# Optimization experiments

Hardware: AMD Instinct MI355X
Metric: run time of the kernel (lower is better)

Reference implementation:

```python
import jax, jax.numpy as jnp
import numpy as np

B, S_NEW, DIM = 32, 1, 4096
H, KV, HD = 32, 8, 128          # query heads, kv heads, head_dim
PREV = 2048                      # tokens already in the KV cache


def setup_inputs() -> dict:
    key = jax.random.key(0)
    ks = jax.random.split(key, 8)
    return {
        "x": jax.random.normal(ks[0], (B, S_NEW, DIM), jnp.float32),
        "wq": jax.random.normal(ks[1], (DIM, H * HD), jnp.float32) * 0.02,
        "wk": jax.random.normal(ks[2], (DIM, KV * HD), jnp.float32) * 0.02,
        "wv": jax.random.normal(ks[3], (DIM, KV * HD), jnp.float32) * 0.02,
        "wo": jax.random.normal(ks[4], (H * HD, DIM), jnp.float32) * 0.02,
        "cache_k": jax.random.normal(ks[5], (B, PREV, KV, HD), jnp.float32),
        "cache_v": jax.random.normal(ks[6], (B, PREV, KV, HD), jnp.float32),
        "freqs": jax.random.normal(ks[7], (S_NEW, HD // 2), jnp.float32),  # rotary angles (angle of freqs_cis)
    }


def _apply_rope(t, cos, sin):
    # t: [b, s, h, hd]; interleaved pairs as in torch.view_as_complex
    a = t[..., 0::2]
    b = t[..., 1::2]
    c = cos[None, :, None, :]
    s = sin[None, :, None, :]
    ra = a * c - b * s
    rb = a * s + b * c
    return jnp.stack([ra, rb], axis=-1).reshape(t.shape)


def reference(x, wq, wk, wv, wo, cache_k, cache_v, freqs):
    b, s, _ = x.shape  # s == 1 (decode)
    xq = (x @ wq).reshape(b, s, H, HD)
    xk = (x @ wk).reshape(b, s, KV, HD)
    xv = (x @ wv).reshape(b, s, KV, HD)

    cos, sin = jnp.cos(freqs), jnp.sin(freqs)
    xq = _apply_rope(xq, cos, sin)
    xk = _apply_rope(xk, cos, sin)

    # KV-cache append (update_cache_decode)
    k_full = jnp.concatenate([cache_k, xk], axis=1)  # [b, PREV+1, KV, hd]
    v_full = jnp.concatenate([cache_v, xv], axis=1)

    # GQA attention without materializing the expanded cache
    g = H // KV
    q = xq.reshape(b, KV, g, HD)  # s == 1 folded away
    scale = 1.0 / jnp.sqrt(jnp.asarray(HD, x.dtype))
    scores = jnp.einsum("bkgd,bskd->bkgs", q, k_full) * scale  # [b, KV, g, PREV+1]
    attn = jax.nn.softmax(scores, axis=-1)
    out = jnp.einsum("bkgs,bskd->bkgd", attn, v_full)  # [b, KV, g, hd]
    out = out.reshape(b, s, H * HD)
    return out @ wo
```

## Files before the change

kernel.cpp:

```cpp
#include <hip/hip_runtime.h>


#define WS_P1   0
#define WS_PA   0
#define WS_QKV  6291456
#define WS_ATTN 6488064
#define WS_P2   6619136

__global__ __launch_bounds__(256) void gemm_skinny(
    const float* __restrict__ X,
    const float* __restrict__ W0, int e0, int ld0,
    const float* __restrict__ W1, int e1, int ld1,
    const float* __restrict__ W2, int ld2,
    float* __restrict__ P, int Ntot)
{
    __shared__ float x_t[128][36];
    __shared__ float2 red[128][33];

    const int nb = blockIdx.x * 256;
    const float* W; int ld, noff;
    if (nb < e0)      { W = W0; ld = ld0; noff = 0;  }
    else if (nb < e1) { W = W1; ld = ld1; noff = e0; }
    else              { W = W2; ld = ld2; noff = e1; }

    const int k0  = blockIdx.y * 128;
    const int tid = threadIdx.x;
    const int cp  = tid & 127;
    const int kg  = tid >> 7;
    const int nn  = nb - noff + cp * 2;

    #pragma unroll
    for (int i = 0; i < 16; ++i) {
        int idx = tid + i * 256;
        int bb = idx >> 7, kk = idx & 127;
        x_t[kk][bb] = X[(size_t)bb * 4096 + k0 + kk];
    }
    __syncthreads();

    float2 acc[32];
    #pragma unroll
    for (int b = 0; b < 32; ++b) { acc[b].x = 0.f; acc[b].y = 0.f; }

    const float* Wp = W + (size_t)k0 * ld + nn;
    for (int kk0 = kg * 64; kk0 < kg * 64 + 64; kk0 += 8) {
        float2 w[8];
        #pragma unroll
        for (int u = 0; u < 8; ++u)
            w[u] = *(const float2*)&Wp[(size_t)(kk0 + u) * ld];
        #pragma unroll
        for (int u = 0; u < 8; ++u) {
            const float* xr = x_t[kk0 + u];
            #pragma unroll
            for (int bq = 0; bq < 8; ++bq) {
                float4 xv = *(const float4*)&xr[bq * 4];
                acc[bq*4+0].x += xv.x * w[u].x; acc[bq*4+0].y += xv.x * w[u].y;
                acc[bq*4+1].x += xv.y * w[u].x; acc[bq*4+1].y += xv.y * w[u].y;
                acc[bq*4+2].x += xv.z * w[u].x; acc[bq*4+2].y += xv.z * w[u].y;
                acc[bq*4+3].x += xv.w * w[u].x; acc[bq*4+3].y += xv.w * w[u].y;
            }
        }
    }

    if (kg == 1) {
        #pragma unroll
        for (int b = 0; b < 32; ++b) red[cp][b] = acc[b];
    }
    __syncthreads();
    if (kg == 0) {
        const int ks = blockIdx.y;
        #pragma unroll
        for (int b = 0; b < 32; ++b) {
            float2 o = red[cp][b];
            float2 v; v.x = acc[b].x + o.x; v.y = acc[b].y + o.y;
            *(float2*)&P[((size_t)ks * 32 + b) * Ntot + nb + cp * 2] = v;
        }
    }
}

__global__ __launch_bounds__(128) void reduce_rope(
    const float* __restrict__ P, const float* __restrict__ freqs,
    float* __restrict__ qkv)
{
    int t = blockIdx.x * 128 + threadIdx.x;
    int b = t / 3072;
    int cp = t - b * 3072;
    int n = cp * 2;
    float sx = 0.f, sy = 0.f;
    #pragma unroll
    for (int ks = 0; ks < 32; ++ks) {
        float2 v = *(const float2*)&P[((size_t)ks * 32 + b) * 6144 + n];
        sx += v.x; sy += v.y;
    }
    if (n < 5120) {
        int d = n & 127;
        float fr = freqs[d >> 1];
        float c = cosf(fr), s = sinf(fr);
        float ra = sx * c - sy * s;
        float rb = sx * s + sy * c;
        if (n < 4096) {
            const float sc = 0.08838834764831845f;
            ra *= sc; rb *= sc;
        }
        sx = ra; sy = rb;
    }
    float2 o; o.x = sx; o.y = sy;
    *(float2*)&qkv[(size_t)b * 6144 + n] = o;
}

__global__ __launch_bounds__(256, 8) void attn_split(
    const float* __restrict__ qkv,
    const float* __restrict__ ck, const float* __restrict__ cv,
    float* __restrict__ pa)
{
    __shared__ float sbuf[4096];
    __shared__ float pm[4], pl[4];

    const int blk = blockIdx.x;
    const int c   = blk & 7;
    const int kv  = (blk >> 3) & 7;
    const int b   = blk >> 6;
    const int tid = threadIdx.x;
    const int wave = tid >> 6, lane = tid & 63;
    const int psub = (lane >> 4) & 3, dl = lane & 15;
    const int s0 = c * 256;
    const bool last = (c == 7);

    float q[4][8];
    {
        const float* qb = qkv + (size_t)b * 6144 + kv * 512 + dl * 8;
        #pragma unroll
        for (int h = 0; h < 4; ++h) {
            float4 a = *(const float4*)&qb[h * 128];
            float4 e = *(const float4*)&qb[h * 128 + 4];
            q[h][0]=a.x; q[h][1]=a.y; q[h][2]=a.z; q[h][3]=a.w;
            q[h][4]=e.x; q[h][5]=e.y; q[h][6]=e.z; q[h][7]=e.w;
        }
    }

    if (last && tid < 16) {
        const float* kr = qkv + (size_t)b * 6144 + 4096 + kv * 128 + dl * 8;
        float4 k0 = *(const float4*)kr;
        float4 k1 = *(const float4*)(kr + 4);
        float p[4];
        #pragma unroll
        for (int h = 0; h < 4; ++h) {
            p[h] = q[h][0]*k0.x + q[h][1]*k0.y + q[h][2]*k0.z + q[h][3]*k0.w
                 + q[h][4]*k1.x + q[h][5]*k1.y + q[h][6]*k1.z + q[h][7]*k1.w;
        }
        #pragma unroll
        for (int off = 1; off < 16; off <<= 1) {
            #pragma unroll
            for (int h = 0; h < 4; ++h) p[h] += __shfl_xor(p[h], off);
        }
        if (dl == 0) {
            #pragma unroll
            for (int h = 0; h < 4; ++h) sbuf[h * 260 + 256] = p[h];
        }
    }

    const float* kbase = ck + (((size_t)b * 2048 + s0) * 8 + kv) * 128;
    const int srow = wave * 4 + psub;
    for (int it0 = 0; it0 < 16; it0 += 4) {
        float4 kA[4][2];
        #pragma unroll
        for (int u = 0; u < 4; ++u) {
            const float* kr = kbase + (size_t)((it0 + u) * 16 + srow) * 1024 + dl * 8;
            kA[u][0] = *(const float4*)kr;
            kA[u][1] = *(const float4*)(kr + 4);
        }
        #pragma unroll
        for (int u = 0; u < 4; ++u) {
            int s = (it0 + u) * 16 + srow;
            float p[4];
            #pragma unroll
            for (int h = 0; h < 4; ++h) {
                p[h] = q[h][0]*kA[u][0].x + q[h][1]*kA[u][0].y
                     + q[h][2]*kA[u][0].z + q[h][3]*kA[u][0].w
                     + q[h][4]*kA[u][1].x + q[h][5]*kA[u][1].y
                     + q[h][6]*kA[u][1].z + q[h][7]*kA[u][1].w;
            }
            #pragma unroll
            for (int off = 1; off < 16; off <<= 1) {
                #pragma unroll
                for (int h = 0; h < 4; ++h) p[h] += __shfl_xor(p[h], off);
            }
            if (dl == 0) {
                #pragma unroll
                for (int h = 0; h < 4; ++h) sbuf[h * 260 + s] = p[h];
            }
        }
    }
    __syncthreads();

    {
        const int h = wave;
        const int nrow = last ? 257 : 256;
        float m = -1e30f;
        for (int s = lane; s < nrow; s += 64) m = fmaxf(m, sbuf[h * 260 + s]);
        #pragma unroll
        for (int off = 1; off < 64; off <<= 1) m = fmaxf(m, __shfl_xor(m, off));
        float sum = 0.f;
        for (int s = lane; s < nrow; s += 64) {
            float p = __expf(sbuf[h * 260 + s] - m);
            sbuf[h * 260 + s] = p;
            sum += p;
        }
        #pragma unroll
        for (int off = 1; off < 64; off <<= 1) sum += __shfl_xor(sum, off);
        if (lane == 0) { pm[h] = m; pl[h] = sum; }
    }
    __syncthreads();

    const int grp = tid >> 5, l32 = tid & 31, d4 = l32 * 4;
    float4 acc[4];
    #pragma unroll
    for (int hh = 0; hh < 4; ++hh) { acc[hh].x=0.f; acc[hh].y=0.f; acc[hh].z=0.f; acc[hh].w=0.f; }
    const float* vbase = cv + (((size_t)b * 2048 + s0) * 8 + kv) * 128;
    for (int it = 0; it < 8; ++it) {
        float4 vv[4];
        float pp[4][4];
        #pragma unroll
        for (int j = 0; j < 4; ++j) {
            int s = it * 32 + j * 8 + grp;
            vv[j] = *(const float4*)&vbase[(size_t)s * 1024 + d4];
        }
        #pragma unroll
        for (int j = 0; j < 4; ++j) {
            int s = it * 32 + j * 8 + grp;
            #pragma unroll
            for (int hh = 0; hh < 4; ++hh) pp[j][hh] = sbuf[hh * 260 + s];
        }
        #pragma unroll
        for (int j = 0; j < 4; ++j) {
            #pragma unroll
            for (int hh = 0; hh < 4; ++hh) {
                acc[hh].x += pp[j][hh] * vv[j].x;
                acc[hh].y += pp[j][hh] * vv[j].y;
                acc[hh].z += pp[j][hh] * vv[j].z;
                acc[hh].w += pp[j][hh] * vv[j].w;
            }
        }
    }
    if (last && grp == 0) {
        const float* vr = qkv + (size_t)b * 6144 + 5120 + kv * 128;
        float4 v = *(const float4*)&vr[d4];
        #pragma unroll
        for (int hh = 0; hh < 4; ++hh) {
            float p = sbuf[hh * 260 + 256];
            acc[hh].x += p * v.x; acc[hh].y += p * v.y;
            acc[hh].z += p * v.z; acc[hh].w += p * v.w;
        }
    }
    __syncthreads();

    #pragma unroll
    for (int hh = 0; hh < 4; ++hh)
        *(float4*)&sbuf[grp * 512 + hh * 128 + d4] = acc[hh];
    __syncthreads();

    float* rec = pa + (size_t)blk * 520;
    for (int t = tid; t < 512; t += 256) {
        int hh = t >> 7, d = t & 127;
        float v = 0.f;
        #pragma unroll
        for (int g = 0; g < 8; ++g) v += sbuf[g * 512 + hh * 128 + d];
        rec[8 + hh * 128 + d] = v;
    }
    if (tid < 4) { rec[tid] = pm[tid]; rec[4 + tid] = pl[tid]; }
}

__global__ __launch_bounds__(128) void attn_combine(
    const float* __restrict__ pa, float* __restrict__ ao)
{
    __shared__ float w_[8][4];
    const int g = blockIdx.x;
    const int b = g >> 3, kv = g & 7;
    const int d = threadIdx.x;
    const float* base = pa + (size_t)(b * 64 + kv * 8) * 520;

    if (d < 4) {
        float M = -1e30f;
        #pragma unroll
        for (int c = 0; c < 8; ++c)
            M = fmaxf(M, base[(size_t)c * 520 + d]);
        float L = 0.f;
        float e[8];
        #pragma unroll
        for (int c = 0; c < 8; ++c) {
            e[c] = __expf(base[(size_t)c * 520 + d] - M);
            L += base[(size_t)c * 520 + 4 + d] * e[c];
        }
        float inv = 1.0f / L;
        #pragma unroll
        for (int c = 0; c < 8; ++c) w_[c][d] = e[c] * inv;
    }
    __syncthreads();

    #pragma unroll
    for (int h = 0; h < 4; ++h) {
        float v = 0.f;
        #pragma unroll
        for (int c = 0; c < 8; ++c)
            v += base[(size_t)c * 520 + 8 + h * 128 + d] * w_[c][h];
        ao[(size_t)g * 512 + h * 128 + d] = v;
    }
}

__global__ __launch_bounds__(128) void reduce_out(
    const float* __restrict__ P, float* __restrict__ out)
{
    int t = blockIdx.x * 128 + threadIdx.x;
    int b = t >> 11;
    int cp = t & 2047;
    int n = cp * 2;
    float sx = 0.f, sy = 0.f;
    #pragma unroll
    for (int ks = 0; ks < 32; ++ks) {
        float2 v = *(const float2*)&P[((size_t)ks * 32 + b) * 4096 + n];
        sx += v.x; sy += v.y;
    }
    float2 o; o.x = sx; o.y = sy;
    *(float2*)&out[(size_t)b * 4096 + n] = o;
}

extern "C" void kernel_launch(void* const* d_in, const int* in_sizes, int n_in,
                              void* d_out, int out_size, void* d_ws, size_t ws_size,
                              hipStream_t stream) {
    const float* x  = (const float*)d_in[0];
    const float* wq = (const float*)d_in[1];
    const float* wk = (const float*)d_in[2];
    const float* wv = (const float*)d_in[3];
    const float* wo = (const float*)d_in[4];
    const float* ck = (const float*)d_in[5];
    const float* cv = (const float*)d_in[6];
    const float* fr = (const float*)d_in[7];
    float* out = (float*)d_out;
    float* ws  = (float*)d_ws;

    float* P1   = ws + WS_P1;
    float* PA   = ws + WS_PA;
    float* qkv  = ws + WS_QKV;
    float* attn = ws + WS_ATTN;
    float* P2   = ws + WS_P2;

    dim3 g1(24, 32);
    gemm_skinny<<<g1, 256, 0, stream>>>(x, wq, 4096, 4096, wk, 5120, 1024,
                                        wv, 1024, P1, 6144);
    reduce_rope<<<768, 128, 0, stream>>>(P1, fr, qkv);
    attn_split<<<2048, 256, 0, stream>>>(qkv, ck, cv, PA);
    attn_combine<<<256, 128, 0, stream>>>(PA, attn);
    dim3 g4(16, 32);
    gemm_skinny<<<g4, 256, 0, stream>>>(attn, wo, 4096, 4096, wo, 4096, 4096,
                                        wo, 4096, P2, 4096);
    reduce_out<<<512, 128, 0, stream>>>(P2, out);
}
```

Before: 216.7 us.

## Split fused attention into separate scores, softmax and PV kernels

Replaces the single split-KV attention kernel, which did online softmax per chunk and rescaled chunks in the combine step, with three kernels. The first writes raw QK scores to global memory over finer chunks, the second computes the exact global softmax per (batch, kv-head) and stores its normalisation, and the third does the PV accumulation, scaled by the stored inverse sum. This simplifies the combine step and gives the scores kernel more parallelism. The cost is two extra kernel launches and an extra round trip of scores through global memory.

```diff
diff --git a/kernel.cpp b/kernel.cpp
--- a/kernel.cpp
+++ b/kernel.cpp
@@ -2,10 +2,12 @@
 
 
 #define WS_P1   0
-#define WS_PA   0
 #define WS_QKV  6291456
 #define WS_ATTN 6488064
 #define WS_P2   6619136
+#define WS_SC   10813440
+#define WS_LINV 12914688
+#define WS_PA   12915712
 
 __global__ __launch_bounds__(256) void gemm_skinny(
     const float* __restrict__ X,
@@ -107,23 +109,19 @@
     *(float2*)&qkv[(size_t)b * 6144 + n] = o;
 }
 
-__global__ __launch_bounds__(256, 8) void attn_split(
+__global__ __launch_bounds__(256) void attn_scores(
     const float* __restrict__ qkv,
-    const float* __restrict__ ck, const float* __restrict__ cv,
-    float* __restrict__ pa)
-{
-    __shared__ float sbuf[4096];
-    __shared__ float pm[4], pl[4];
-
+    const float* __restrict__ ck,
+    float* __restrict__ sc)
+{
     const int blk = blockIdx.x;
-    const int c   = blk & 7;
-    const int kv  = (blk >> 3) & 7;
-    const int b   = blk >> 6;
+    const int c   = blk & 15;
+    const int kv  = (blk >> 4) & 7;
+    const int b   = blk >> 7;
     const int tid = threadIdx.x;
     const int wave = tid >> 6, lane = tid & 63;
     const int psub = (lane >> 4) & 3, dl = lane & 15;
-    const int s0 = c * 256;
-    const bool last = (c == 7);
+    const int s0 = c * 128;
 
     float q[4][8];
     {
@@ -137,40 +135,20 @@
         }
     }
 
-    if (last && tid < 16) {
-        const float* kr = qkv + (size_t)b * 6144 + 4096 + kv * 128 + dl * 8;
-        float4 k0 = *(const float4*)kr;
-        float4 k1 = *(const float4*)(kr + 4);
-        float p[4];
-        #pragma unroll
-        for (int h = 0; h < 4; ++h) {
-            p[h] = q[h][0]*k0.x + q[h][1]*k0.y + q[h][2]*k0.z + q[h][3]*k0.w
-                 + q[h][4]*k1.x + q[h][5]*k1.y + q[h][6]*k1.z + q[h][7]*k1.w;
-        }
-        #pragma unroll
-        for (int off = 1; off < 16; off <<= 1) {
-            #pragma unroll
-            for (int h = 0; h < 4; ++h) p[h] += __shfl_xor(p[h], off);
-        }
-        if (dl == 0) {
-            #pragma unroll
-            for (int h = 0; h < 4; ++h) sbuf[h * 260 + 256] = p[h];
-        }
-    }
-
+    float* scb = sc + (size_t)(b * 8 + kv) * 8208;
     const float* kbase = ck + (((size_t)b * 2048 + s0) * 8 + kv) * 128;
     const int srow = wave * 4 + psub;
-    for (int it0 = 0; it0 < 16; it0 += 4) {
-        float4 kA[4][2];
-        #pragma unroll
-        for (int u = 0; u < 4; ++u) {
+
+    for (int it0 = 0; it0 < 8; it0 += 2) {
+        float4 kA[2][2];
+        #pragma unroll
+        for (int u = 0; u < 2; ++u) {
             const float* kr = kbase + (size_t)((it0 + u) * 16 + srow) * 1024 + dl * 8;
             kA[u][0] = *(const float4*)kr;
             kA[u][1] = *(const float4*)(kr + 4);
         }
         #pragma unroll
-        for (int u = 0; u < 4; ++u) {
-            int s = (it0 + u) * 16 + srow;
+        for (int u = 0; u < 2; ++u) {
             float p[4];
             #pragma unroll
             for (int h = 0; h < 4; ++h) {
@@ -185,124 +163,184 @@
                 for (int h = 0; h < 4; ++h) p[h] += __shfl_xor(p[h], off);
             }
             if (dl == 0) {
-                #pragma unroll
-                for (int h = 0; h < 4; ++h) sbuf[h * 260 + s] = p[h];
+                int s = s0 + (it0 + u) * 16 + srow;
+                float4 o; o.x = p[0]; o.y = p[1]; o.z = p[2]; o.w = p[3];
+                *(float4*)&scb[(size_t)s * 4] = o;
             }
         }
     }
-    __syncthreads();
-
-    {
-        const int h = wave;
-        const int nrow = last ? 257 : 256;
-        float m = -1e30f;
-        for (int s = lane; s < nrow; s += 64) m = fmaxf(m, sbuf[h * 260 + s]);
-        #pragma unroll
-        for (int off = 1; off < 64; off <<= 1) m = fmaxf(m, __shfl_xor(m, off));
-        float sum = 0.f;
-        for (int s = lane; s < nrow; s += 64) {
-            float p = __expf(sbuf[h * 260 + s] - m);
-            sbuf[h * 260 + s] = p;
-            sum += p;
-        }
-        #pragma unroll
-        for (int off = 1; off < 64; off <<= 1) sum += __shfl_xor(sum, off);
-        if (lane == 0) { pm[h] = m; pl[h] = sum; }
-    }
-    __syncthreads();
-
+
+    if (c == 15 && wave == 0 && psub == 0) {
+        const float* kr = qkv + (size_t)b * 6144 + 4096 + kv * 128 + dl * 8;
+        float4 k0 = *(const float4*)kr;
+        float4 k1 = *(const float4*)(kr + 4);
+        float p[4];
+        #pragma unroll
+        for (int h = 0; h < 4; ++h) {
+            p[h] = q[h][0]*k0.x + q[h][1]*k0.y + q[h][2]*k0.z + q[h][3]*k0.w
+                 + q[h][4]*k1.x + q[h][5]*k1.y + q[h][6]*k1.z + q[h][7]*k1.w;
+        }
+        #pragma unroll
+        for (int off = 1; off < 16; off <<= 1) {
+            #pragma unroll
+            for (int h = 0; h < 4; ++h) p[h] += __shfl_xor(p[h], off);
+        }
+        if (dl == 0) {
+            float4 o; o.x = p[0]; o.y = p[1]; o.z = p[2]; o.w = p[3];
+            *(float4*)&scb[(size_t)2048 * 4] = o;
+        }
+    }
+}
+
+__global__ __launch_bounds__(256) void attn_softmax(
+    float* __restrict__ sc, float* __restrict__ linv)
+{
+    __shared__ float red[4][4];
+    const int g = blockIdx.x;
+    float* scb = sc + (size_t)g * 8208;
+    const int tid = threadIdx.x;
+    const int wave = tid >> 6, lane = tid & 63;
+
+    float4 m4; m4.x = -1e30f; m4.y = -1e30f; m4.z = -1e30f; m4.w = -1e30f;
+    for (int s = tid; s < 2049; s += 256) {
+        float4 v = *(const float4*)&scb[(size_t)s * 4];
+        m4.x = fmaxf(m4.x, v.x); m4.y = fmaxf(m4.y, v.y);
+        m4.z = fmaxf(m4.z, v.z); m4.w = fmaxf(m4.w, v.w);
+    }
+    #pragma unroll
+    for (int off = 1; off < 64; off <<= 1) {
+        m4.x = fmaxf(m4.x, __shfl_xor(m4.x, off));
+        m4.y = fmaxf(m4.y, __shfl_xor(m4.y, off));
+        m4.z = fmaxf(m4.z, __shfl_xor(m4.z, off));
+        m4.w = fmaxf(m4.w, __shfl_xor(m4.w, off));
+    }
+    if (lane == 0) {
+        red[wave][0] = m4.x; red[wave][1] = m4.y;
+        red[wave][2] = m4.z; red[wave][3] = m4.w;
+    }
+    __syncthreads();
+    float4 M;
+    M.x = fmaxf(fmaxf(red[0][0], red[1][0]), fmaxf(red[2][0], red[3][0]));
+    M.y = fmaxf(fmaxf(red[0][1], red[1][1]), fmaxf(red[2][1], red[3][1]));
+    M.z = fmaxf(fmaxf(red[0][2], red[1][2]), fmaxf(red[2][2], red[3][2]));
+    M.w = fmaxf(fmaxf(red[0][3], red[1][3]), fmaxf(red[2][3], red[3][3]));
+    __syncthreads();
+
+    float4 l4; l4.x = 0.f; l4.y = 0.f; l4.z = 0.f; l4.w = 0.f;
+    for (int s = tid; s < 2049; s += 256) {
+        float4 v = *(const float4*)&scb[(size_t)s * 4];
+        v.x = __expf(v.x - M.x); v.y = __expf(v.y - M.y);
+        v.z = __expf(v.z - M.z); v.w = __expf(v.w - M.w);
+        *(float4*)&scb[(size_t)s * 4] = v;
+        l4.x += v.x; l4.y += v.y; l4.z += v.z; l4.w += v.w;
+    }
+    #pragma unroll
+    for (int off = 1; off < 64; off <<= 1) {
+        l4.x += __shfl_xor(l4.x, off);
+        l4.y += __shfl_xor(l4.y, off);
+        l4.z += __shfl_xor(l4.z, off);
+        l4.w += __shfl_xor(l4.w, off);
+    }
+    if (lane == 0) {
+        red[wave][0] = l4.x; red[wave][1] = l4.y;
+        red[wave][2] = l4.z; red[wave][3] = l4.w;
+    }
+    __syncthreads();
+    if (tid < 4) {
+        float L = red[0][tid] + red[1][tid] + red[2][tid] + red[3][tid];
+        linv[(size_t)g * 4 + tid] = 1.0f / L;
+    }
+}
+
+__global__ __launch_bounds__(256) void attn_pv(
+    const float* __restrict__ qkv, const float* __restrict__ cv,
+    const float* __restrict__ sc, const float* __restrict__ linv,
+    float* __restrict__ pa)
+{
+    __shared__ float sbuf[8][512];
+    const int blk = blockIdx.x;
+    const int c   = blk & 7;
+    const int kv  = (blk >> 3) & 7;
+    const int b   = blk >> 6;
+    const int tid = threadIdx.x;
     const int grp = tid >> 5, l32 = tid & 31, d4 = l32 * 4;
+    const int s0 = c * 256;
+
+    const float* scb = sc + (size_t)(b * 8 + kv) * 8208;
+    const float* vbase = cv + (((size_t)b * 2048 + s0) * 8 + kv) * 128;
+
     float4 acc[4];
     #pragma unroll
-    for (int hh = 0; hh < 4; ++hh) { acc[hh].x=0.f; acc[hh].y=0.f; acc[hh].z=0.f; acc[hh].w=0.f; }
-    const float* vbase = cv + (((size_t)b * 2048 + s0) * 8 + kv) * 128;
+    for (int h = 0; h < 4; ++h) { acc[h].x=0.f; acc[h].y=0.f; acc[h].z=0.f; acc[h].w=0.f; }
+
     for (int it = 0; it < 8; ++it) {
         float4 vv[4];
-        float pp[4][4];
+        float4 pj[4];
         #pragma unroll
         for (int j = 0; j < 4; ++j) {
-            int s = it * 32 + j * 8 + grp;
-            vv[j] = *(const float4*)&vbase[(size_t)s * 1024 + d4];
+            int sl = it * 32 + j * 8 + grp;
+            vv[j] = *(const float4*)&vbase[(size_t)sl * 1024 + d4];
         }
         #pragma unroll
         for (int j = 0; j < 4; ++j) {
-            int s = it * 32 + j * 8 + grp;
-            #pragma unroll
-            for (int hh = 0; hh < 4; ++hh) pp[j][hh] = sbuf[hh * 260 + s];
+            int sl = it * 32 + j * 8 + grp;
+            pj[j] = *(const float4*)&scb[(size_t)(s0 + sl) * 4];
         }
         #pragma unroll
         for (int j = 0; j < 4; ++j) {
-            #pragma unroll
-            for (int hh = 0; hh < 4; ++hh) {
-                acc[hh].x += pp[j][hh] * vv[j].x;
-                acc[hh].y += pp[j][hh] * vv[j].y;
-                acc[hh].z += pp[j][hh] * vv[j].z;
-                acc[hh].w += pp[j][hh] * vv[j].w;
-            }
-        }
-    }
-    if (last && grp == 0) {
+            acc[0].x += pj[j].x * vv[j].x; acc[0].y += pj[j].x * vv[j].y;
+            acc[0].z += pj[j].x * vv[j].z; acc[0].w += pj[j].x * vv[j].w;
+            acc[1].x += pj[j].y * vv[j].x; acc[1].y += pj[j].y * vv[j].y;
+            acc[1].z += pj[j].y * vv[j].z; acc[1].w += pj[j].y * vv[j].w;
+            acc[2].x += pj[j].z * vv[j].x; acc[2].y += pj[j].z * vv[j].y;
+            acc[2].z += pj[j].z * vv[j].z; acc[2].w += pj[j].z * vv[j].w;
+            acc[3].x += pj[j].w * vv[j].x; acc[3].y += pj[j].w * vv[j].y;
+            acc[3].z += pj[j].w * vv[j].z; acc[3].w += pj[j].w * vv[j].w;
+        }
+    }
+    if (c == 7 && grp == 0) {
         const float* vr = qkv + (size_t)b * 6144 + 5120 + kv * 128;
         float4 v = *(const float4*)&vr[d4];
-        #pragma unroll
-        for (int hh = 0; hh < 4; ++hh) {
-            float p = sbuf[hh * 260 + 256];
-            acc[hh].x += p * v.x; acc[hh].y += p * v.y;
-            acc[hh].z += p * v.z; acc[hh].w += p * v.w;
-        }
-    }
-    __syncthreads();
-
-    #pragma unroll
-    for (int hh = 0; hh < 4; ++hh)
-        *(float4*)&sbuf[grp * 512 + hh * 128 + d4] = acc[hh];
-    __syncthreads();
-
-    float* rec = pa + (size_t)blk * 520;
+        float4 p = *(const float4*)&scb[(size_t)2048 * 4];
+        acc[0].x += p.x * v.x; acc[0].y += p.x * v.y; acc[0].z += p.x * v.z; acc[0].w += p.x * v.w;
+        acc[1].x += p.y * v.x; acc[1].y += p.y * v.y; acc[1].z += p.y * v.z; acc[1].w += p.y * v.w;
+        acc[2].x += p.z * v.x; acc[2].y += p.z * v.y; acc[2].z += p.z * v.z; acc[2].w += p.z * v.w;
+        acc[3].x += p.w * v.x; acc[3].y += p.w * v.y; acc[3].z += p.w * v.z; acc[3].w += p.w * v.w;
+    }
+
+    {
+        float4 li = *(const float4*)&linv[(size_t)(b * 8 + kv) * 4];
+        acc[0].x *= li.x; acc[0].y *= li.x; acc[0].z *= li.x; acc[0].w *= li.x;
+        acc[1].x *= li.y; acc[1].y *= li.y; acc[1].z *= li.y; acc[1].w *= li.y;
+        acc[2].x *= li.z; acc[2].y *= li.z; acc[2].z *= li.z; acc[2].w *= li.z;
+        acc[3].x *= li.w; acc[3].y *= li.w; acc[3].z *= li.w; acc[3].w *= li.w;
+    }
+    #pragma unroll
+    for (int h = 0; h < 4; ++h)
+        *(float4*)&sbuf[grp][h * 128 + d4] = acc[h];
+    __syncthreads();
+
+    float* rec = pa + (size_t)blk * 512;
     for (int t = tid; t < 512; t += 256) {
-        int hh = t >> 7, d = t & 127;
         float v = 0.f;
         #pragma unroll
-        for (int g = 0; g < 8; ++g) v += sbuf[g * 512 + hh * 128 + d];
-        rec[8 + hh * 128 + d] = v;
-    }
-    if (tid < 4) { rec[tid] = pm[tid]; rec[4 + tid] = pl[tid]; }
+        for (int g2 = 0; g2 < 8; ++g2) v += sbuf[g2][t];
+        rec[t] = v;
+    }
 }
 
 __global__ __launch_bounds__(128) void attn_combine(
     const float* __restrict__ pa, float* __restrict__ ao)
 {
-    __shared__ float w_[8][4];
     const int g = blockIdx.x;
-    const int b = g >> 3, kv = g & 7;
     const int d = threadIdx.x;
-    const float* base = pa + (size_t)(b * 64 + kv * 8) * 520;
-
-    if (d < 4) {
-        float M = -1e30f;
-        #pragma unroll
-        for (int c = 0; c < 8; ++c)
-            M = fmaxf(M, base[(size_t)c * 520 + d]);
-        float L = 0.f;
-        float e[8];
-        #pragma unroll
-        for (int c = 0; c < 8; ++c) {
-            e[c] = __expf(base[(size_t)c * 520 + d] - M);
-            L += base[(size_t)c * 520 + 4 + d] * e[c];
-        }
-        float inv = 1.0f / L;
-        #pragma unroll
-        for (int c = 0; c < 8; ++c) w_[c][d] = e[c] * inv;
-    }
-    __syncthreads();
-
+    const float* base = pa + (size_t)g * 8 * 512;
     #pragma unroll
     for (int h = 0; h < 4; ++h) {
         float v = 0.f;
         #pragma unroll
-        for (int c = 0; c < 8; ++c)
-            v += base[(size_t)c * 520 + 8 + h * 128 + d] * w_[c][h];
-        ao[(size_t)g * 512 + h * 128 + d] = v;
+        for (int c = 0; c < 8; ++c) v += base[c * 512 + h * 128 + d];
+        ao[(size_t)(g >> 3) * 4096 + (g & 7) * 512 + h * 128 + d] = v;
     }
 }
 
@@ -338,16 +376,20 @@
     float* ws  = (float*)d_ws;
 
     float* P1   = ws + WS_P1;
-    float* PA   = ws + WS_PA;
     float* qkv  = ws + WS_QKV;
     float* attn = ws + WS_ATTN;
     float* P2   = ws + WS_P2;
+    float* SC   = ws + WS_SC;
+    float* LINV = ws + WS_LINV;
+    float* PA   = ws + WS_PA;
 
     dim3 g1(24, 32);
     gemm_skinny<<<g1, 256, 0, stream>>>(x, wq, 4096, 4096, wk, 5120, 1024,
                                         wv, 1024, P1, 6144);
     reduce_rope<<<768, 128, 0, stream>>>(P1, fr, qkv);
-    attn_split<<<2048, 256, 0, stream>>>(qkv, ck, cv, PA);
+    attn_scores<<<4096, 256, 0, stream>>>(qkv, ck, SC);
+    attn_softmax<<<256, 256, 0, stream>>>(SC, LINV);
+    attn_pv<<<2048, 256, 0, stream>>>(qkv, cv, SC, LINV, PA);
     attn_combine<<<256, 128, 0, stream>>>(PA, attn);
     dim3 g4(16, 32);
     gemm_skinny<<<g4, 256, 0, stream>>>(attn, wo, 4096, 4096, wo, 4096, 4096,
```

After: 207.3 us. 1.05x faster.
